# Performance work log

Hardware: AMD Instinct MI355X
Metric: run time of the kernel (lower is better)

Reference implementation:

```python
import jax, jax.numpy as jnp
import numpy as np

NUM_HEADS = 16
HIDDEN = 1024
HEAD_DIM = HIDDEN // NUM_HEADS
BS, SEQ = 2, 2048


def setup_inputs() -> dict:
    key = jax.random.key(0)
    ks = jax.random.split(key, 9)
    s = 1.0 / np.sqrt(HIDDEN)
    return {
        "Q": jax.random.normal(ks[0], (BS, SEQ, HIDDEN), jnp.float32),
        "K": jax.random.normal(ks[1], (BS, SEQ, HIDDEN), jnp.float32),
        "V": jax.random.normal(ks[2], (BS, SEQ, HIDDEN), jnp.float32),
        "attention_mask": jnp.zeros((BS, 1, 1, SEQ), jnp.float32),
        # nn.Linear weights stored as [in, out] (already transposed)
        "Wq": jax.random.uniform(ks[3], (HIDDEN, HIDDEN), jnp.float32, -s, s),
        "bq": jax.random.uniform(ks[4], (HIDDEN,), jnp.float32, -s, s),
        "Wk": jax.random.uniform(ks[5], (HIDDEN, HIDDEN), jnp.float32, -s, s),
        "bk": jax.random.uniform(ks[6], (HIDDEN,), jnp.float32, -s, s),
        "Wv": jax.random.uniform(ks[7], (HIDDEN, HIDDEN), jnp.float32, -s, s),
        "bv": jax.random.uniform(ks[8], (HIDDEN,), jnp.float32, -s, s),
    }


def _split_heads(x):
    b, s, _ = x.shape
    return x.reshape(b, s, NUM_HEADS, HEAD_DIM).transpose(0, 2, 1, 3)  # [b,h,s,d]


def reference(Q, K, V, attention_mask, Wq, bq, Wk, bk, Wv, bv):
    q = _split_heads(Q @ Wq + bq)  # [b,h,s,d]
    k = _split_heads(K @ Wk + bk)
    v = _split_heads(V @ Wv + bv)
    score = jnp.einsum("bhqd,bhkd->bhqk", q, k)
    # NOTE: original adds mask BEFORE scaling by 1/sqrt(d)
    score = (score + attention_mask) / np.sqrt(HEAD_DIM)
    attn = jax.nn.softmax(score, axis=-1)
    out = jnp.einsum("bhqk,bhkd->bqhd", attn, v)  # [b,q,h,d]
    b, s = Q.shape[:2]
    return out.reshape(b, s, NUM_HEADS * HEAD_DIM)
```

## Files before the change

### kernel.cpp

```cpp
#include <hip/hip_runtime.h>
#include <hip/hip_bf16.h>
#include <stdint.h>

#define SEQ    2048
#define HIDDEN 1024
#define NH     16
#define HD     64

#define SC_LOG2E_8 0.18033688011112042f
#define SM_SHIFT   16.0f

typedef __bf16 bf16x8 __attribute__((ext_vector_type(8)));
typedef float  f32x4  __attribute__((ext_vector_type(4)));
typedef float  f32x16 __attribute__((ext_vector_type(16)));
typedef unsigned int uint32x2 __attribute__((ext_vector_type(2)));

typedef __attribute__((address_space(1))) void* as1vp;
typedef __attribute__((address_space(3))) void* as3vp;

__device__ __forceinline__ void gload_lds16(const void* g, void* l) {
  __builtin_amdgcn_global_load_lds((as1vp)(void*)g, (as3vp)l, 16, 0, 0);
}

__device__ __forceinline__ uint16_t f2bf(float f) {
  uint32_t x;
  __builtin_memcpy(&x, &f, 4);
  x += 0x7FFFu + ((x >> 16) & 1u);
  return (uint16_t)(x >> 16);
}

__device__ __forceinline__ uint32_t pkbf(float lo, float hi) {
  union { __bf16 v[2]; uint32_t u; } t;
  t.v[0] = (__bf16)lo; t.v[1] = (__bf16)hi;
  return t.u;
}

__device__ __forceinline__ uint32x2 plswap(uint32_t lo, uint32_t hi) {
  return __builtin_amdgcn_permlane32_swap(lo, hi, false, false);
}

__device__ __forceinline__ float xhalf32(float x, int lane) {
  uint32_t a;
  __builtin_memcpy(&a, &x, 4);
  uint32x2 r = plswap(a, a);
  uint32_t p = (lane < 32) ? r[1] : r[0];
  float f;
  __builtin_memcpy(&f, &p, 4);
  return f;
}

__device__ __forceinline__ float exp2_fast(float x) {
  return __builtin_amdgcn_exp2f(x);
}

__global__ __launch_bounds__(256) void k_cvt(
    const float* __restrict__ Q, const float* __restrict__ K, const float* __restrict__ V,
    const float* __restrict__ mask,
    uint16_t* __restrict__ Qb, uint16_t* __restrict__ Kb, uint16_t* __restrict__ Vb,
    float* __restrict__ mask_sc) {
  if (blockIdx.x == 2048) {
    if (blockIdx.y < 2) {
      const int i = (blockIdx.y * 256 + threadIdx.x) * 8;
      float4 a = *(const float4*)(mask + i);
      float4 b = *(const float4*)(mask + i + 4);
      a.x = a.x * SC_LOG2E_8 - SM_SHIFT; a.y = a.y * SC_LOG2E_8 - SM_SHIFT;
      a.z = a.z * SC_LOG2E_8 - SM_SHIFT; a.w = a.w * SC_LOG2E_8 - SM_SHIFT;
      b.x = b.x * SC_LOG2E_8 - SM_SHIFT; b.y = b.y * SC_LOG2E_8 - SM_SHIFT;
      b.z = b.z * SC_LOG2E_8 - SM_SHIFT; b.w = b.w * SC_LOG2E_8 - SM_SHIFT;
      *(float4*)(mask_sc + i) = a;
      *(float4*)(mask_sc + i + 4) = b;
    }
    return;
  }
  const float* src = (blockIdx.y == 0) ? Q : (blockIdx.y == 1) ? K : V;
  uint16_t*    dst = (blockIdx.y == 0) ? Qb : (blockIdx.y == 1) ? Kb : Vb;
  const int i = (blockIdx.x * 256 + threadIdx.x) * 8;
  float4 v0 = *(const float4*)(src + i);
  float4 v1 = *(const float4*)(src + i + 4);
  uint16_t tmp[8];
  tmp[0] = f2bf(v0.x); tmp[1] = f2bf(v0.y); tmp[2] = f2bf(v0.z); tmp[3] = f2bf(v0.w);
  tmp[4] = f2bf(v1.x); tmp[5] = f2bf(v1.y); tmp[6] = f2bf(v1.z); tmp[7] = f2bf(v1.w);
  __builtin_memcpy(dst + i, tmp, 16);
}

__global__ __launch_bounds__(256) void k_transpose(
    const float* __restrict__ W0, const float* __restrict__ W1, const float* __restrict__ W2,
    uint16_t* __restrict__ T0, uint16_t* __restrict__ T1, uint16_t* __restrict__ T2) {
  __shared__ uint16_t t[64][65];
  const float* W = (blockIdx.y == 0) ? W0 : (blockIdx.y == 1) ? W1 : W2;
  uint16_t*    T = (blockIdx.y == 0) ? T0 : (blockIdx.y == 1) ? T1 : T2;
  const int bx = blockIdx.x & 15, by = blockIdx.x >> 4;
  const int tx = threadIdx.x & 63, ty = threadIdx.x >> 6;
  for (int i = ty; i < 64; i += 4)
    t[i][tx] = f2bf(W[(by * 64 + i) * HIDDEN + bx * 64 + tx]);
  __syncthreads();
  for (int i = ty; i < 64; i += 4)
    T[(bx * 64 + i) * HIDDEN + by * 64 + tx] = t[tx][i];
}

__global__ __launch_bounds__(256) void k_qkv_gemm(
    const uint16_t* __restrict__ Qb, const uint16_t* __restrict__ Kb, const uint16_t* __restrict__ Vb,
    const uint16_t* __restrict__ WTq, const uint16_t* __restrict__ WTk, const uint16_t* __restrict__ WTv,
    const float* __restrict__ Bq, const float* __restrict__ Bk, const float* __restrict__ Bv,
    uint16_t* __restrict__ q_ws, uint16_t* __restrict__ k_ws, uint16_t* __restrict__ v_ws) {
  const int wg  = blockIdx.x;
  const int swz = (wg & 7) * 96 + (wg >> 3);
  const int mode = swz >> 8;
  const int rem  = swz & 255;
  const int m0   = (rem >> 3) * 128;
  const int n0   = (rem & 7) * 128;

  const uint16_t* X   = (mode == 0) ? Qb : (mode == 1) ? Kb : Vb;
  const uint16_t* WT  = (mode == 0) ? WTq : (mode == 1) ? WTk : WTv;
  const float*    bia = (mode == 0) ? Bq  : (mode == 1) ? Bk  : Bv;

  __shared__ uint16_t As[128 * 64];
  __shared__ uint16_t Bs[128 * 64];
  char* AsB = (char*)As;
  char* BsB = (char*)Bs;

  const int tid  = threadIdx.x;
  const int lane = tid & 63;
  const int w    = tid >> 6;
  const int wr   = w >> 1, wc = w & 1;

  const int lrow = lane >> 3;
  const int lcol = (lane & 7) * 16;

  f32x4 acc[4][4];
  const f32x4 zero = {0.f, 0.f, 0.f, 0.f};
#pragma unroll
  for (int i = 0; i < 4; ++i)
#pragma unroll
    for (int j = 0; j < 4; ++j) acc[i][j] = zero;

  const char* Ab = (const char*)X;
  const char* Bb = (const char*)WT;

  for (int kt = 0; kt < 16; ++kt) {
    __syncthreads();
    const int kbyte = kt * 128;
#pragma unroll
    for (int i = 0; i < 4; ++i) {
      const int r = w * 32 + i * 8;
      gload_lds16(Ab + (size_t)(m0 + r + lrow) * (HIDDEN * 2) + kbyte + lcol, AsB + r * 128);
      gload_lds16(Bb + (size_t)(n0 + r + lrow) * (HIDDEN * 2) + kbyte + lcol, BsB + r * 128);
    }
    __syncthreads();
#pragma unroll
    for (int kc = 0; kc < 2; ++kc) {
      const int chunk = kc * 64 + (lane >> 4) * 16;
      bf16x8 a[4], b[4];
#pragma unroll
      for (int f = 0; f < 4; ++f) {
        const int ra = wr * 64 + f * 16 + (lane & 15);
        a[f] = *(const bf16x8*)(AsB + ra * 128 + chunk);
        const int rb = wc * 64 + f * 16 + (lane & 15);
        b[f] = *(const bf16x8*)(BsB + rb * 128 + chunk);
      }
#pragma unroll
      for (int fm = 0; fm < 4; ++fm)
#pragma unroll
        for (int fn = 0; fn < 4; ++fn)
          acc[fm][fn] = __builtin_amdgcn_mfma_f32_16x16x32_bf16(a[fm], b[fn], acc[fm][fn], 0, 0, 0);
    }
  }

  float bfrag[4];
#pragma unroll
  for (int fn = 0; fn < 4; ++fn)
    bfrag[fn] = bia[n0 + wc * 64 + fn * 16 + (lane & 15)];

#pragma unroll
  for (int fm = 0; fm < 4; ++fm) {
    const int mrow0 = m0 + wr * 64 + fm * 16 + (lane >> 4) * 4;
    const int b0 = mrow0 >> 11;
    const int sq = mrow0 & (SEQ - 1);
#pragma unroll
    for (int fn = 0; fn < 4; ++fn) {
      const int n = n0 + wc * 64 + fn * 16 + (lane & 15);
      const int h = n >> 6, d = n & 63;
      const size_t bh = (size_t)(b0 * NH + h);
      if (mode == 2) {
        const int kt2 = sq >> 6, ks = (sq >> 4) & 3, hv = (sq >> 3) & 1, jj = sq & 7;
        const int dt = d >> 5, lnv = hv * 32 + (d & 31);
        uint16_t tmp[4];
#pragma unroll
        for (int j = 0; j < 4; ++j) tmp[j] = f2bf(acc[fm][fn][j] + bfrag[fn]);
        __builtin_memcpy(v_ws + ((((bh * 32 + kt2) * 2 + dt) * 4 + ks) * 64 + lnv) * 8 + jj,
                         tmp, 8);
      } else if (mode == 1) {
        const int kt2 = sq >> 6, c = (sq >> 5) & 1, ql = sq & 31;
        const int slot = d >> 4, hk = (d >> 3) & 1, jk = d & 7;
        uint16_t* base = k_ws + ((((bh * 32 + kt2) * 2 + c) * 4 + slot) * 64 + hk * 32 + ql) * 8 + jk;
#pragma unroll
        for (int j = 0; j < 4; ++j) base[j * 8] = f2bf(acc[fm][fn][j] + bfrag[fn]);
      } else {
        const int qt32 = sq >> 5, ql = sq & 31;
        const int slot = d >> 4, hq = (d >> 3) & 1, jq = d & 7;
        uint16_t* base = q_ws + (((bh * 64 + qt32) * 4 + slot) * 64 + hq * 32 + ql) * 8 + jq;
#pragma unroll
        for (int j = 0; j < 4; ++j)
          base[j * 8] = f2bf((acc[fm][fn][j] + bfrag[fn]) * SC_LOG2E_8);
      }
    }
  }
}

__global__ __launch_bounds__(256) void k_attn(
    const uint16_t* __restrict__ q_ws, const uint16_t* __restrict__ k_ws,
    const uint16_t* __restrict__ v_ws, const float* __restrict__ mask_sc,
    float* __restrict__ out) {
  __shared__ float smem[3][64][33];

  const int tid = threadIdx.x, lane = tid & 63, w = tid >> 6;
  const int wg  = blockIdx.x;
  const int swz = (wg & 7) * 256 + (wg >> 3);
  const int bh  = swz >> 6;
  const int qt  = swz & 63;
  const int b   = bh >> 4;
  const int h   = bh & 15;
  const int q0  = qt * 32;
  const int ql  = lane & 31;
  const int hi  = lane >> 5;

  const char* qfb = (const char*)q_ws + ((size_t)bh * 64 + qt) * 4096;
  const char* kfb = (const char*)k_ws + (size_t)bh * 262144 + lane * 16;
  const char* vfb = (const char*)v_ws + (size_t)bh * 262144 + lane * 16;
  const float* mrow = mask_sc + b * SEQ;

  bf16x8 qB[4];
#pragma unroll
  for (int s = 0; s < 4; ++s)
    qB[s] = *(const bf16x8*)(qfb + s * 1024 + lane * 16);

  const f32x16 zero16 = {0.f};
  f32x16 Oacc[2];
  Oacc[0] = zero16; Oacc[1] = zero16;
  float lpart = 0.f;

  const int kbeg = w * 8, kend = kbeg + 8;

  for (int kt = kbeg; kt < kend; ++kt) {
    const char* kt_k = kfb + (size_t)kt * 8192;
    const char* kt_v = vfb + (size_t)kt * 8192;

    bf16x8 kf[8];
#pragma unroll
    for (int i = 0; i < 8; ++i) kf[i] = *(const bf16x8*)(kt_k + i * 1024);

    f32x16 P0, P1;
#pragma unroll
    for (int g = 0; g < 4; ++g) {
      f32x4 mk0 = *(const f32x4*)(mrow + kt * 64 + g * 8 + 4 * hi);
      f32x4 mk1 = *(const f32x4*)(mrow + kt * 64 + 32 + g * 8 + 4 * hi);
#pragma unroll
      for (int t = 0; t < 4; ++t) { P0[g * 4 + t] = mk0[t]; P1[g * 4 + t] = mk1[t]; }
    }

#pragma unroll
    for (int s = 0; s < 4; ++s)
      P0 = __builtin_amdgcn_mfma_f32_32x32x16_bf16(kf[s], qB[s], P0, 0, 0, 0);
#pragma unroll
    for (int s = 0; s < 4; ++s)
      P1 = __builtin_amdgcn_mfma_f32_32x32x16_bf16(kf[4 + s], qB[s], P1, 0, 0, 0);

    bf16x8 vA[8];
#pragma unroll
    for (int i = 0; i < 8; ++i) vA[i] = *(const bf16x8*)(kt_v + i * 1024);

    float s0 = 0.f, s1 = 0.f, s2a = 0.f, s3 = 0.f;
#pragma unroll
    for (int r = 0; r < 16; r += 4) {
      P0[r]     = exp2_fast(P0[r]);      s0  += P0[r];
      P0[r + 1] = exp2_fast(P0[r + 1]);  s1  += P0[r + 1];
      P0[r + 2] = exp2_fast(P0[r + 2]);  s2a += P0[r + 2];
      P0[r + 3] = exp2_fast(P0[r + 3]);  s3  += P0[r + 3];
      P1[r]     = exp2_fast(P1[r]);      s0  += P1[r];
      P1[r + 1] = exp2_fast(P1[r + 1]);  s1  += P1[r + 1];
      P1[r + 2] = exp2_fast(P1[r + 2]);  s2a += P1[r + 2];
      P1[r + 3] = exp2_fast(P1[r + 3]);  s3  += P1[r + 3];
    }
    lpart += (s0 + s1) + (s2a + s3);

    bf16x8 pb[4];
#pragma unroll
    for (int ks = 0; ks < 4; ++ks) {
      const int o = (ks & 1) * 8;
      uint32_t w0, w1, w2, w3;
      if (ks < 2) {
        w0 = pkbf(P0[o + 0], P0[o + 1]);
        w1 = pkbf(P0[o + 2], P0[o + 3]);
        w2 = pkbf(P0[o + 4], P0[o + 5]);
        w3 = pkbf(P0[o + 6], P0[o + 7]);
      } else {
        w0 = pkbf(P1[o + 0], P1[o + 1]);
        w1 = pkbf(P1[o + 2], P1[o + 3]);
        w2 = pkbf(P1[o + 4], P1[o + 5]);
        w3 = pkbf(P1[o + 6], P1[o + 7]);
      }
      uint32x2 r02 = plswap(w0, w2);
      uint32x2 r13 = plswap(w1, w3);
      uint32_t wv[4] = {r02[0], r13[0], r02[1], r13[1]};
      __builtin_memcpy(&pb[ks], wv, 16);
    }

#pragma unroll
    for (int ks = 0; ks < 4; ++ks) {
      Oacc[0] = __builtin_amdgcn_mfma_f32_32x32x16_bf16(vA[ks],     pb[ks], Oacc[0], 0, 0, 0);
      Oacc[1] = __builtin_amdgcn_mfma_f32_32x32x16_bf16(vA[4 + ks], pb[ks], Oacc[1], 0, 0, 0);
    }
  }

  if (w > 0) {
    float* s = smem[w - 1][lane];
#pragma unroll
    for (int r = 0; r < 16; ++r) { s[r] = Oacc[0][r]; s[16 + r] = Oacc[1][r]; }
    s[32] = lpart;
  }
  __syncthreads();
  if (w > 0) return;

#pragma unroll
  for (int p = 0; p < 3; ++p) {
    const float* s = smem[p][lane];
#pragma unroll
    for (int r = 0; r < 16; ++r) { Oacc[0][r] += s[r]; Oacc[1][r] += s[16 + r]; }
    lpart += s[32];
  }

  const float ltot = lpart + xhalf32(lpart, lane);
  const float linv = 1.f / ltot;
  float* orow = out + ((size_t)(b * SEQ) + q0 + ql) * HIDDEN + h * HD;
#pragma unroll
  for (int dt = 0; dt < 2; ++dt)
#pragma unroll
    for (int g = 0; g < 4; ++g) {
      f32x4 o;
#pragma unroll
      for (int t = 0; t < 4; ++t) o[t] = Oacc[dt][g * 4 + t] * linv;
      *(f32x4*)(orow + dt * 32 + g * 8 + 4 * hi) = o;
    }
}

extern "C" void kernel_launch(void* const* d_in, const int* in_sizes, int n_in,
                              void* d_out, int out_size, void* d_ws, size_t ws_size,
                              hipStream_t stream) {
  (void)in_sizes; (void)n_in; (void)out_size; (void)ws_size;
  const float* Q    = (const float*)d_in[0];
  const float* K    = (const float*)d_in[1];
  const float* V    = (const float*)d_in[2];
  const float* mask = (const float*)d_in[3];
  const float* Wq   = (const float*)d_in[4];
  const float* bq   = (const float*)d_in[5];
  const float* Wk   = (const float*)d_in[6];
  const float* bk   = (const float*)d_in[7];
  const float* Wv   = (const float*)d_in[8];
  const float* bv   = (const float*)d_in[9];

  uint16_t* ws   = (uint16_t*)d_ws;
  uint16_t* wt_q = ws;
  uint16_t* wt_k = wt_q + HIDDEN * HIDDEN;
  uint16_t* wt_v = wt_k + HIDDEN * HIDDEN;
  const size_t qkv = (size_t)2 * SEQ * HIDDEN;
  uint16_t* Qb   = wt_v + HIDDEN * HIDDEN;
  uint16_t* Kb   = Qb + qkv;
  uint16_t* Vb   = Kb + qkv;
  uint16_t* q_ws = Vb + qkv;
  uint16_t* k_ws = q_ws + qkv;
  uint16_t* v_ws = k_ws + qkv;
  float* mask_sc = (float*)(v_ws + qkv);

  k_cvt<<<dim3(2049, 3), 256, 0, stream>>>(Q, K, V, mask, Qb, Kb, Vb, mask_sc);
  k_transpose<<<dim3(256, 3), 256, 0, stream>>>(Wq, Wk, Wv, wt_q, wt_k, wt_v);
  k_qkv_gemm<<<dim3(768), 256, 0, stream>>>(
      Qb, Kb, Vb, wt_q, wt_k, wt_v, bq, bk, bv, q_ws, k_ws, v_ws);
  k_attn<<<dim3(2048), 256, 0, stream>>>(q_ws, k_ws, v_ws, mask_sc,
                                         (float*)d_out);
}
```

Baseline: 133.3 us.

## Share K/V tiles across four query waves via double-buffered LDS staging

The attention kernel now gives each wave its own 32-row query tile, so a workgroup covers 128 queries instead of splitting the key range of one 32-row tile across four waves. K and V tiles are loaded cooperatively into double-buffered LDS using global_load_lds, so all four waves reuse them, and the cross-wave reduction at the end is removed. This cuts global and L2 traffic for K/V by roughly four times and removes the final LDS reduction. In exchange it adds a barrier every key tile, makes each wave's serial loop four times longer, and launches four times fewer workgroups (512), which may underfill the GPU.

```diff
diff --git a/kernel.cpp b/kernel.cpp
--- a/kernel.cpp
+++ b/kernel.cpp
@@ -211,22 +211,22 @@
     const uint16_t* __restrict__ q_ws, const uint16_t* __restrict__ k_ws,
     const uint16_t* __restrict__ v_ws, const float* __restrict__ mask_sc,
     float* __restrict__ out) {
-  __shared__ float smem[3][64][33];
+  __shared__ char lds[2][16384];
 
   const int tid = threadIdx.x, lane = tid & 63, w = tid >> 6;
   const int wg  = blockIdx.x;
-  const int swz = (wg & 7) * 256 + (wg >> 3);
-  const int bh  = swz >> 6;
-  const int qt  = swz & 63;
+  const int swz = (wg & 7) * 64 + (wg >> 3);
+  const int bh  = swz >> 4;
+  const int qt  = swz & 15;
   const int b   = bh >> 4;
   const int h   = bh & 15;
-  const int q0  = qt * 32;
+  const int q0  = qt * 128 + w * 32;
   const int ql  = lane & 31;
   const int hi  = lane >> 5;
 
-  const char* qfb = (const char*)q_ws + ((size_t)bh * 64 + qt) * 4096;
-  const char* kfb = (const char*)k_ws + (size_t)bh * 262144 + lane * 16;
-  const char* vfb = (const char*)v_ws + (size_t)bh * 262144 + lane * 16;
+  const char* qfb = (const char*)q_ws + ((size_t)bh * 64 + (q0 >> 5)) * 4096;
+  const char* kgb = (const char*)k_ws + (size_t)bh * 262144 + w * 2048 + lane * 16;
+  const char* vgb = (const char*)v_ws + (size_t)bh * 262144 + w * 2048 + lane * 16;
   const float* mrow = mask_sc + b * SEQ;
 
   bf16x8 qB[4];
@@ -239,15 +239,26 @@
   Oacc[0] = zero16; Oacc[1] = zero16;
   float lpart = 0.f;
 
-  const int kbeg = w * 8, kend = kbeg + 8;
-
-  for (int kt = kbeg; kt < kend; ++kt) {
-    const char* kt_k = kfb + (size_t)kt * 8192;
-    const char* kt_v = vfb + (size_t)kt * 8192;
-
-    bf16x8 kf[8];
-#pragma unroll
-    for (int i = 0; i < 8; ++i) kf[i] = *(const bf16x8*)(kt_k + i * 1024);
+  auto stage = [&](int buf, int kt) {
+    const char* gk = kgb + (size_t)kt * 8192;
+    const char* gv = vgb + (size_t)kt * 8192;
+    char* l = &lds[buf][w * 2048];
+#pragma unroll
+    for (int i = 0; i < 2; ++i) {
+      gload_lds16(gk + i * 1024, l + i * 1024);
+      gload_lds16(gv + i * 1024, l + 8192 + i * 1024);
+    }
+  };
+
+  stage(0, 0);
+  __syncthreads();
+
+  int cur = 0;
+  for (int kt = 0; kt < 32; ++kt) {
+    if (kt + 1 < 32) stage(cur ^ 1, kt + 1);
+
+    const char* lk = &lds[cur][0];
+    const char* lv = &lds[cur][8192];
 
     f32x16 P0, P1;
 #pragma unroll
@@ -258,6 +269,10 @@
       for (int t = 0; t < 4; ++t) { P0[g * 4 + t] = mk0[t]; P1[g * 4 + t] = mk1[t]; }
     }
 
+    bf16x8 kf[8];
+#pragma unroll
+    for (int i = 0; i < 8; ++i) kf[i] = *(const bf16x8*)(lk + i * 1024 + lane * 16);
+
 #pragma unroll
     for (int s = 0; s < 4; ++s)
       P0 = __builtin_amdgcn_mfma_f32_32x32x16_bf16(kf[s], qB[s], P0, 0, 0, 0);
@@ -267,7 +282,7 @@
 
     bf16x8 vA[8];
 #pragma unroll
-    for (int i = 0; i < 8; ++i) vA[i] = *(const bf16x8*)(kt_v + i * 1024);
+    for (int i = 0; i < 8; ++i) vA[i] = *(const bf16x8*)(lv + i * 1024 + lane * 16);
 
     float s0 = 0.f, s1 = 0.f, s2a = 0.f, s3 = 0.f;
 #pragma unroll
@@ -310,23 +325,9 @@
       Oacc[0] = __builtin_amdgcn_mfma_f32_32x32x16_bf16(vA[ks],     pb[ks], Oacc[0], 0, 0, 0);
       Oacc[1] = __builtin_amdgcn_mfma_f32_32x32x16_bf16(vA[4 + ks], pb[ks], Oacc[1], 0, 0, 0);
     }
-  }
-
-  if (w > 0) {
-    float* s = smem[w - 1][lane];
-#pragma unroll
-    for (int r = 0; r < 16; ++r) { s[r] = Oacc[0][r]; s[16 + r] = Oacc[1][r]; }
-    s[32] = lpart;
-  }
-  __syncthreads();
-  if (w > 0) return;
-
-#pragma unroll
-  for (int p = 0; p < 3; ++p) {
-    const float* s = smem[p][lane];
-#pragma unroll
-    for (int r = 0; r < 16; ++r) { Oacc[0][r] += s[r]; Oacc[1][r] += s[16 + r]; }
-    lpart += s[32];
+
+    __syncthreads();
+    cur ^= 1;
   }
 
   const float ltot = lpart + xhalf32(lpart, lane);
@@ -375,6 +376,6 @@
   k_transpose<<<dim3(256, 3), 256, 0, stream>>>(Wq, Wk, Wv, wt_q, wt_k, wt_v);
   k_qkv_gemm<<<dim3(768), 256, 0, stream>>>(
       Qb, Kb, Vb, wt_q, wt_k, wt_v, bq, bk, bv, q_ws, k_ws, v_ws);
-  k_attn<<<dim3(2048), 256, 0, stream>>>(q_ws, k_ws, v_ws, mask_sc,
-                                         (float*)d_out);
-}
+  k_attn<<<dim3(512), 256, 0, stream>>>(q_ws, k_ws, v_ws, mask_sc,
+                                        (float*)d_out);
+}
```

Result: no change. 131.1 us (-1.6%).
